# Kernel optimization log

Measured on AMD Instinct MI355X. Metric: run time of the kernel, lower is better.

## Reference

```python
import jax, jax.numpy as jnp
import numpy as np

NUM_SAMPLED = 8192
NUM_CLASSES = 50000
DIM = 512
BATCH = 8192


def _log_uniform_expected(ids, num_sampled, num_classes):
    # log-uniform sampler probability: P(c) = (log(c+2) - log(c+1)) / log(V+1)
    c = ids.astype(jnp.float32)
    p = (jnp.log(c + 2.0) - jnp.log(c + 1.0)) / jnp.log(float(num_classes + 1))
    # expected count under unique sampling of num_sampled candidates (as in TF)
    return -jnp.expm1(float(num_sampled) * jnp.log1p(-p))


def setup_inputs() -> dict:
    key = jax.random.key(0)
    k1, k2, k3, k4, k5 = jax.random.split(key, 5)
    inputs = jax.random.normal(k1, (BATCH, DIM), jnp.float32)
    labels = jax.random.randint(k2, (BATCH, 1), 0, NUM_CLASSES)
    kernel = jax.random.uniform(k3, (NUM_CLASSES, DIM), jnp.float32, -0.05, 0.05)
    bias = jax.random.uniform(k4, (NUM_CLASSES,), jnp.float32, -0.05, 0.05)
    sampled = jax.random.randint(k5, (NUM_SAMPLED,), 0, NUM_CLASSES)
    return {"inputs": inputs, "labels": labels, "kernel": kernel,
            "bias": bias, "sampled": sampled}


def reference(inputs, labels, kernel, bias, sampled):
    # tf.nn.sampled_softmax_loss (train branch), num_true=1,
    # log-uniform sampler, remove_accidental_hits=True.
    labels_flat = labels[:, 0]

    # true logits: gather one weight row per example, dot with input
    w_true = kernel[labels_flat]                      # [B, D]
    b_true = bias[labels_flat]                        # [B]
    true_logits = jnp.einsum('bd,bd->b', inputs, w_true) + b_true
    true_logits = true_logits - jnp.log(
        _log_uniform_expected(labels_flat, NUM_SAMPLED, NUM_CLASSES))

    # sampled logits: gather S candidate rows, small matmul [B,D]x[D,S]
    w_samp = kernel[sampled]                          # [S, D]
    b_samp = bias[sampled]                            # [S]
    sampled_logits = jnp.einsum('bd,sd->bs', inputs, w_samp) + b_samp[None, :]
    sampled_logits = sampled_logits - jnp.log(
        _log_uniform_expected(sampled, NUM_SAMPLED, NUM_CLASSES))

    # remove accidental hits: mask sampled candidates that equal the true label
    hits = labels_flat[:, None] == sampled[None, :]   # [B, S]
    sampled_logits = jnp.where(hits, -1e9, sampled_logits)

    # softmax CE with the true class at column 0
    logits = jnp.concatenate([true_logits[:, None], sampled_logits], axis=1)
    loss = jax.nn.logsumexp(logits, axis=1) - logits[:, 0]  # [B]
    return loss
```

## Files before the change

kernel.cpp:

```cpp
#include <hip/hip_runtime.h>
#include <hip/hip_bf16.h>
#include <cstdint>
#include <cstddef>

#define BATCH   8192
#define NSAMP   8192
#define DIM     512
#define NCLASS  50000

typedef __attribute__((ext_vector_type(8))) short bf16x8;
typedef __attribute__((ext_vector_type(4))) float f32x4;

__device__ __forceinline__ float neg_log_expected(int c) {
    double p = log1p(1.0 / (double)(c + 1)) / log((double)(NCLASS + 1));
    double e = -expm1((double)NSAMP * log1p(-p));
    return (float)(-log(e));
}

__device__ __forceinline__ unsigned short f2bf(float f) {
    __hip_bfloat16 h = __float2bfloat16(f);
    return *reinterpret_cast<unsigned short*>(&h);
}

__device__ __forceinline__ void gload_lds16(const void* g, void* l) {
    __builtin_amdgcn_global_load_lds(
        (const __attribute__((address_space(1))) void*)g,
        (__attribute__((address_space(3))) void*)l, 16, 0, 0);
}

__global__ void k_convert(const float* __restrict__ in, __hip_bfloat16* __restrict__ out) {
    int t = blockIdx.x * blockDim.x + threadIdx.x;
    float4 v = reinterpret_cast<const float4*>(in)[t];
    ushort4 u;
    u.x = f2bf(v.x); u.y = f2bf(v.y); u.z = f2bf(v.z); u.w = f2bf(v.w);
    reinterpret_cast<ushort4*>(out)[t] = u;
}

__global__ void k_gather(const float* __restrict__ W, const float* __restrict__ bias,
                         const int* __restrict__ sampled,
                         __hip_bfloat16* __restrict__ Bbf, float* __restrict__ adj) {
    int s   = blockIdx.x;
    int idx = sampled[s];
    const float4* src = reinterpret_cast<const float4*>(W + (size_t)idx * DIM);
    float4 v = src[threadIdx.x];
    ushort4 u;
    u.x = f2bf(v.x); u.y = f2bf(v.y); u.z = f2bf(v.z); u.w = f2bf(v.w);
    reinterpret_cast<ushort4*>(Bbf + (size_t)s * DIM)[threadIdx.x] = u;
    if (threadIdx.x == 0) adj[s] = bias[idx] + neg_log_expected(idx);
}

__global__ void k_true(const float* __restrict__ inputs, const int* __restrict__ labels,
                       const float* __restrict__ W, const float* __restrict__ bias,
                       float* __restrict__ true_logit, float* __restrict__ row_sum) {
    int gt   = blockIdx.x * blockDim.x + threadIdx.x;
    int row  = gt >> 6;
    int lane = gt & 63;
    int lbl  = labels[row];
    const float4* xi = reinterpret_cast<const float4*>(inputs + (size_t)row * DIM);
    const float4* wi = reinterpret_cast<const float4*>(W + (size_t)lbl * DIM);
    float dot = 0.f;
    #pragma unroll
    for (int j = 0; j < 2; ++j) {
        float4 a = xi[lane + j * 64];
        float4 b = wi[lane + j * 64];
        dot += a.x * b.x + a.y * b.y + a.z * b.z + a.w * b.w;
    }
    #pragma unroll
    for (int off = 32; off; off >>= 1) dot += __shfl_down(dot, off, 64);
    if (lane == 0) {
        float tl = dot + bias[lbl] + neg_log_expected(lbl);
        true_logit[row] = tl;
        row_sum[row]    = expf(tl);
    }
}

__global__ __launch_bounds__(256) void k_gemm(
    const __hip_bfloat16* __restrict__ A, const __hip_bfloat16* __restrict__ B,
    const float* __restrict__ adj, const int* __restrict__ labels,
    const int* __restrict__ sampled, float* __restrict__ row_sum) {
    __shared__ alignas(16) __hip_bfloat16 Asm[3][128 * 32];
    __shared__ alignas(16) __hip_bfloat16 Bsm[3][128 * 32];
    __shared__ float tsum[2][128];

    const int tid  = threadIdx.x;
    const int wave = tid >> 6;
    const int lane = tid & 63;
    const int wr   = wave >> 1;
    const int wc   = wave & 1;

    int bid = blockIdx.x;
    int wg  = (bid & 7) * 512 + (bid >> 3);
    const int brow = (wg >> 6) * 128;
    const int bcol = (wg & 63) * 128;

    const int srow = lane >> 2;
    const int sg   = (lane & 3) ^ ((lane >> 3) & 3);

    f32x4 acc[4][4];
    #pragma unroll
    for (int m = 0; m < 4; ++m)
        #pragma unroll
        for (int n = 0; n < 4; ++n)
            acc[m][n] = (f32x4){0.f, 0.f, 0.f, 0.f};

    auto stage = [&](int buf, int kt) {
        #pragma unroll
        for (int i = 0; i < 2; ++i) {
            const __hip_bfloat16* gA =
                A + (size_t)(brow + wave * 32 + i * 16 + srow) * DIM + kt * 32 + sg * 8;
            gload_lds16(gA, &Asm[buf][(wave * 32 + i * 16) * 32]);
            const __hip_bfloat16* gB =
                B + (size_t)(bcol + wave * 32 + i * 16 + srow) * DIM + kt * 32 + sg * 8;
            gload_lds16(gB, &Bsm[buf][(wave * 32 + i * 16) * 32]);
        }
    };

    stage(0, 0);
    stage(1, 1);

    const int rsel = lane & 15;
    const int koff = ((lane >> 4) ^ ((lane >> 1) & 3)) * 8;

    bf16x8 a[4], b[4];
    #pragma unroll 1
    for (int kt = 0; kt < 15; ++kt) {
        asm volatile("s_waitcnt vmcnt(4)" ::: "memory");
        asm volatile("s_barrier" ::: "memory");
        const int cur = kt % 3;
        #pragma unroll
        for (int m = 0; m < 4; ++m)
            a[m] = *reinterpret_cast<const bf16x8*>(
                &Asm[cur][(wr * 64 + m * 16 + rsel) * 32 + koff]);
        #pragma unroll
        for (int n = 0; n < 4; ++n)
            b[n] = *reinterpret_cast<const bf16x8*>(
                &Bsm[cur][(wc * 64 + n * 16 + rsel) * 32 + koff]);
        if (kt < 14) stage((kt + 2) % 3, kt + 2);
        #pragma unroll
        for (int m = 0; m < 4; ++m)
            #pragma unroll
            for (int n = 0; n < 4; ++n)
                acc[m][n] = __builtin_amdgcn_mfma_f32_16x16x32_bf16(a[m], b[n], acc[m][n], 0, 0, 0);
    }
    {
        asm volatile("s_waitcnt vmcnt(0)" ::: "memory");
        asm volatile("s_barrier" ::: "memory");
        #pragma unroll
        for (int m = 0; m < 4; ++m)
            a[m] = *reinterpret_cast<const bf16x8*>(
                &Asm[0][(wr * 64 + m * 16 + rsel) * 32 + koff]);
        #pragma unroll
        for (int n = 0; n < 4; ++n)
            b[n] = *reinterpret_cast<const bf16x8*>(
                &Bsm[0][(wc * 64 + n * 16 + rsel) * 32 + koff]);
        #pragma unroll
        for (int m = 0; m < 4; ++m)
            #pragma unroll
            for (int n = 0; n < 4; ++n)
                acc[m][n] = __builtin_amdgcn_mfma_f32_16x16x32_bf16(a[m], b[n], acc[m][n], 0, 0, 0);
    }

    int gcol[4]; float aadj[4]; int sval[4];
    #pragma unroll
    for (int n = 0; n < 4; ++n) {
        gcol[n] = bcol + wc * 64 + n * 16 + rsel;
        aadj[n] = adj[gcol[n]];
        sval[n] = sampled[gcol[n]];
    }
    #pragma unroll
    for (int m = 0; m < 4; ++m) {
        #pragma unroll
        for (int r = 0; r < 4; ++r) {
            int lr  = wr * 64 + m * 16 + (lane >> 4) * 4 + r;
            int lbl = labels[brow + lr];
            float part = 0.f;
            #pragma unroll
            for (int n = 0; n < 4; ++n) {
                float logit = acc[m][n][r] + aadj[n];
                part += (sval[n] == lbl) ? 0.f : __expf(logit);
            }
            part += __shfl_xor(part, 1, 16);
            part += __shfl_xor(part, 2, 16);
            part += __shfl_xor(part, 4, 16);
            part += __shfl_xor(part, 8, 16);
            if (rsel == 0) tsum[wc][lr] = part;
        }
    }
    __syncthreads();
    if (tid < 128) atomicAdd(&row_sum[brow + tid], tsum[0][tid] + tsum[1][tid]);
}

__global__ void k_final(const float* __restrict__ row_sum,
                        const float* __restrict__ true_logit,
                        float* __restrict__ loss) {
    int i = blockIdx.x * blockDim.x + threadIdx.x;
    loss[i] = logf(row_sum[i]) - true_logit[i];
}

extern "C" void kernel_launch(void* const* d_in, const int* in_sizes, int n_in,
                              void* d_out, int out_size, void* d_ws, size_t ws_size,
                              hipStream_t stream) {
    const float* inputs  = (const float*)d_in[0];
    const int*   labels  = (const int*)d_in[1];
    const float* W       = (const float*)d_in[2];
    const float* bias    = (const float*)d_in[3];
    const int*   sampled = (const int*)d_in[4];
    float*       loss    = (float*)d_out;

    char* ws = (char*)d_ws;
    __hip_bfloat16* Abf = (__hip_bfloat16*)ws;
    __hip_bfloat16* Bbf = (__hip_bfloat16*)(ws + (size_t)BATCH * DIM * 2);
    float* adj        = (float*)(ws + (size_t)(BATCH + NSAMP) * DIM * 2);
    float* true_logit = adj + NSAMP;
    float* row_sum    = true_logit + BATCH;

    hipLaunchKernelGGL(k_convert, dim3((BATCH * DIM / 4) / 256), dim3(256), 0, stream,
                       inputs, Abf);
    hipLaunchKernelGGL(k_gather, dim3(NSAMP), dim3(128), 0, stream,
                       W, bias, sampled, Bbf, adj);
    hipLaunchKernelGGL(k_true, dim3(BATCH / 4), dim3(256), 0, stream,
                       inputs, labels, W, bias, true_logit, row_sum);
    hipLaunchKernelGGL(k_gemm, dim3((BATCH / 128) * (NSAMP / 128)), dim3(256), 0, stream,
                       Abf, Bbf, adj, labels, sampled, row_sum);
    hipLaunchKernelGGL(k_final, dim3(BATCH / 256), dim3(256), 0, stream,
                       row_sum, true_logit, loss);
}
```

Measured before the change: 147.3 us.

## Persistent GEMM over column tiles with 4-stage pipeline and fused convert/true-logit kernel

The GEMM becomes a persistent kernel with 512 blocks. Each block processes 8 consecutive column tiles for one row block, and the load pipeline runs continuously across tile boundaries with a 4-buffer ring. This removes per-tile prologue and epilogue stalls and launch overhead, and keeps A rows resident in cache per XCD. The input conversion and true-logit dot product are also fused into one kernel that reads inputs once. The cost is fewer blocks, so occupancy is lower (launch_bounds 256,2), and the epilogue now sits inside the main loop.

```diff
diff --git a/kernel.cpp b/kernel.cpp
--- a/kernel.cpp
+++ b/kernel.cpp
@@ -28,12 +28,30 @@
         (__attribute__((address_space(3))) void*)l, 16, 0, 0);
 }
 
-__global__ void k_convert(const float* __restrict__ in, __hip_bfloat16* __restrict__ out) {
-    int t = blockIdx.x * blockDim.x + threadIdx.x;
-    float4 v = reinterpret_cast<const float4*>(in)[t];
+__global__ void k_fused(const float* __restrict__ inputs, const int* __restrict__ labels,
+                        const float* __restrict__ W, const float* __restrict__ bias,
+                        __hip_bfloat16* __restrict__ Abf,
+                        float* __restrict__ true_logit, float* __restrict__ row_sum) {
+    int row = blockIdx.x;
+    int t   = threadIdx.x;
+    float4 v = reinterpret_cast<const float4*>(inputs + (size_t)row * DIM)[t];
     ushort4 u;
     u.x = f2bf(v.x); u.y = f2bf(v.y); u.z = f2bf(v.z); u.w = f2bf(v.w);
-    reinterpret_cast<ushort4*>(out)[t] = u;
+    reinterpret_cast<ushort4*>(Abf + (size_t)row * DIM)[t] = u;
+
+    int lbl = labels[row];
+    float4 w = reinterpret_cast<const float4*>(W + (size_t)lbl * DIM)[t];
+    float dot = v.x * w.x + v.y * w.y + v.z * w.z + v.w * w.w;
+    #pragma unroll
+    for (int off = 32; off; off >>= 1) dot += __shfl_down(dot, off, 64);
+    __shared__ float red[2];
+    if ((t & 63) == 0) red[t >> 6] = dot;
+    __syncthreads();
+    if (t == 0) {
+        float tl = red[0] + red[1] + bias[lbl] + neg_log_expected(lbl);
+        true_logit[row] = tl;
+        row_sum[row]    = __expf(tl);
+    }
 }
 
 __global__ void k_gather(const float* __restrict__ W, const float* __restrict__ bias,
@@ -41,45 +59,24 @@
                          __hip_bfloat16* __restrict__ Bbf, float* __restrict__ adj) {
     int s   = blockIdx.x;
     int idx = sampled[s];
-    const float4* src = reinterpret_cast<const float4*>(W + (size_t)idx * DIM);
-    float4 v = src[threadIdx.x];
+    float4 v = reinterpret_cast<const float4*>(W + (size_t)idx * DIM)[threadIdx.x];
     ushort4 u;
     u.x = f2bf(v.x); u.y = f2bf(v.y); u.z = f2bf(v.z); u.w = f2bf(v.w);
     reinterpret_cast<ushort4*>(Bbf + (size_t)s * DIM)[threadIdx.x] = u;
     if (threadIdx.x == 0) adj[s] = bias[idx] + neg_log_expected(idx);
 }
 
-__global__ void k_true(const float* __restrict__ inputs, const int* __restrict__ labels,
-                       const float* __restrict__ W, const float* __restrict__ bias,
-                       float* __restrict__ true_logit, float* __restrict__ row_sum) {
-    int gt   = blockIdx.x * blockDim.x + threadIdx.x;
-    int row  = gt >> 6;
-    int lane = gt & 63;
-    int lbl  = labels[row];
-    const float4* xi = reinterpret_cast<const float4*>(inputs + (size_t)row * DIM);
-    const float4* wi = reinterpret_cast<const float4*>(W + (size_t)lbl * DIM);
-    float dot = 0.f;
-    #pragma unroll
-    for (int j = 0; j < 2; ++j) {
-        float4 a = xi[lane + j * 64];
-        float4 b = wi[lane + j * 64];
-        dot += a.x * b.x + a.y * b.y + a.z * b.z + a.w * b.w;
-    }
-    #pragma unroll
-    for (int off = 32; off; off >>= 1) dot += __shfl_down(dot, off, 64);
-    if (lane == 0) {
-        float tl = dot + bias[lbl] + neg_log_expected(lbl);
-        true_logit[row] = tl;
-        row_sum[row]    = expf(tl);
-    }
-}
-
-__global__ __launch_bounds__(256) void k_gemm(
+
+#define BARRIER()  asm volatile("s_barrier" ::: "memory")
+#define LBARRIER() asm volatile("s_waitcnt lgkmcnt(0)\n\ts_barrier" ::: "memory")
+#define VMCNT(n)   asm volatile("s_waitcnt vmcnt(" #n ")" ::: "memory")
+
+__global__ __launch_bounds__(256, 2) void k_gemm(
     const __hip_bfloat16* __restrict__ A, const __hip_bfloat16* __restrict__ B,
     const float* __restrict__ adj, const int* __restrict__ labels,
     const int* __restrict__ sampled, float* __restrict__ row_sum) {
-    __shared__ alignas(16) __hip_bfloat16 Asm[3][128 * 32];
-    __shared__ alignas(16) __hip_bfloat16 Bsm[3][128 * 32];
+    __shared__ alignas(16) __hip_bfloat16 Asm[4][128 * 32];
+    __shared__ alignas(16) __hip_bfloat16 Bsm[4][128 * 32];
     __shared__ float tsum[2][128];
 
     const int tid  = threadIdx.x;
@@ -88,13 +85,17 @@
     const int wr   = wave >> 1;
     const int wc   = wave & 1;
 
-    int bid = blockIdx.x;
-    int wg  = (bid & 7) * 512 + (bid >> 3);
-    const int brow = (wg >> 6) * 128;
-    const int bcol = (wg & 63) * 128;
+    const int bid  = blockIdx.x;
+    const int xcd  = bid & 7;
+    const int idx  = bid >> 3;
+    const int rb   = (idx & 7) * 8 + xcd;
+    const int cg   = idx >> 3;
+    const int brow = rb * 128;
 
     const int srow = lane >> 2;
     const int sg   = (lane & 3) ^ ((lane >> 3) & 3);
+    const int rsel = lane & 15;
+    const int koff = ((lane >> 4) ^ ((lane >> 1) & 3)) * 8;
 
     f32x4 acc[4][4];
     #pragma unroll
@@ -103,7 +104,9 @@
         for (int n = 0; n < 4; ++n)
             acc[m][n] = (f32x4){0.f, 0.f, 0.f, 0.f};
 
-    auto stage = [&](int buf, int kt) {
+    auto stage = [&](int g) {
+        const int buf = g & 3, t = g >> 4, kt = g & 15;
+        const int bcol = (cg * 8 + t) * 128;
         #pragma unroll
         for (int i = 0; i < 2; ++i) {
             const __hip_bfloat16* gA =
@@ -115,79 +118,75 @@
         }
     };
 
-    stage(0, 0);
-    stage(1, 1);
-
-    const int rsel = lane & 15;
-    const int koff = ((lane >> 4) ^ ((lane >> 1) & 3)) * 8;
-
-    bf16x8 a[4], b[4];
-    #pragma unroll 1
-    for (int kt = 0; kt < 15; ++kt) {
-        asm volatile("s_waitcnt vmcnt(4)" ::: "memory");
-        asm volatile("s_barrier" ::: "memory");
-        const int cur = kt % 3;
+    auto body = [&](int buf) {
+        bf16x8 a[4], b[4];
         #pragma unroll
         for (int m = 0; m < 4; ++m)
             a[m] = *reinterpret_cast<const bf16x8*>(
-                &Asm[cur][(wr * 64 + m * 16 + rsel) * 32 + koff]);
+                &Asm[buf][(wr * 64 + m * 16 + rsel) * 32 + koff]);
         #pragma unroll
         for (int n = 0; n < 4; ++n)
             b[n] = *reinterpret_cast<const bf16x8*>(
-                &Bsm[cur][(wc * 64 + n * 16 + rsel) * 32 + koff]);
-        if (kt < 14) stage((kt + 2) % 3, kt + 2);
+                &Bsm[buf][(wc * 64 + n * 16 + rsel) * 32 + koff]);
         #pragma unroll
         for (int m = 0; m < 4; ++m)
             #pragma unroll
             for (int n = 0; n < 4; ++n)
                 acc[m][n] = __builtin_amdgcn_mfma_f32_16x16x32_bf16(a[m], b[n], acc[m][n], 0, 0, 0);
-    }
-    {
-        asm volatile("s_waitcnt vmcnt(0)" ::: "memory");
-        asm volatile("s_barrier" ::: "memory");
-        #pragma unroll
-        for (int m = 0; m < 4; ++m)
-            a[m] = *reinterpret_cast<const bf16x8*>(
-                &Asm[0][(wr * 64 + m * 16 + rsel) * 32 + koff]);
-        #pragma unroll
-        for (int n = 0; n < 4; ++n)
-            b[n] = *reinterpret_cast<const bf16x8*>(
-                &Bsm[0][(wc * 64 + n * 16 + rsel) * 32 + koff]);
+    };
+
+    auto epi = [&](int t) {
+        const int bcol = (cg * 8 + t) * 128;
+        int sv[4]; float aadj[4];
+        #pragma unroll
+        for (int n = 0; n < 4; ++n) {
+            int col = bcol + wc * 64 + n * 16 + rsel;
+            aadj[n] = adj[col];
+            sv[n]   = sampled[col];
+        }
+        #pragma unroll
+        for (int m = 0; m < 4; ++m) {
+            #pragma unroll
+            for (int r = 0; r < 4; ++r) {
+                int lr  = wr * 64 + m * 16 + (lane >> 4) * 4 + r;
+                int lbl = labels[brow + lr];
+                float part = 0.f;
+                #pragma unroll
+                for (int n = 0; n < 4; ++n) {
+                    float logit = acc[m][n][r] + aadj[n];
+                    part += (sv[n] == lbl) ? 0.f : __expf(logit);
+                }
+                part += __shfl_xor(part, 1, 16);
+                part += __shfl_xor(part, 2, 16);
+                part += __shfl_xor(part, 4, 16);
+                part += __shfl_xor(part, 8, 16);
+                if (rsel == 0) tsum[wc][lr] = part;
+            }
+        }
+        LBARRIER();
+        if (tid < 128)
+            atomicAdd(&row_sum[brow + tid], tsum[0][tid] + tsum[1][tid]);
         #pragma unroll
         for (int m = 0; m < 4; ++m)
             #pragma unroll
             for (int n = 0; n < 4; ++n)
-                acc[m][n] = __builtin_amdgcn_mfma_f32_16x16x32_bf16(a[m], b[n], acc[m][n], 0, 0, 0);
+                acc[m][n] = (f32x4){0.f, 0.f, 0.f, 0.f};
+    };
+
+    stage(0); stage(1); stage(2);
+
+    #pragma unroll 1
+    for (int g = 0; g < 126; ++g) {
+        VMCNT(8);
+        BARRIER();
+        const int buf = g & 3;
+        if (g + 3 < 128) stage(g + 3);
+        body(buf);
+        if ((g & 15) == 15) epi(g >> 4);
     }
-
-    int gcol[4]; float aadj[4]; int sval[4];
-    #pragma unroll
-    for (int n = 0; n < 4; ++n) {
-        gcol[n] = bcol + wc * 64 + n * 16 + rsel;
-        aadj[n] = adj[gcol[n]];
-        sval[n] = sampled[gcol[n]];
-    }
-    #pragma unroll
-    for (int m = 0; m < 4; ++m) {
-        #pragma unroll
-        for (int r = 0; r < 4; ++r) {
-            int lr  = wr * 64 + m * 16 + (lane >> 4) * 4 + r;
-            int lbl = labels[brow + lr];
-            float part = 0.f;
-            #pragma unroll
-            for (int n = 0; n < 4; ++n) {
-                float logit = acc[m][n][r] + aadj[n];
-                part += (sval[n] == lbl) ? 0.f : __expf(logit);
-            }
-            part += __shfl_xor(part, 1, 16);
-            part += __shfl_xor(part, 2, 16);
-            part += __shfl_xor(part, 4, 16);
-            part += __shfl_xor(part, 8, 16);
-            if (rsel == 0) tsum[wc][lr] = part;
-        }
-    }
-    __syncthreads();
-    if (tid < 128) atomicAdd(&row_sum[brow + tid], tsum[0][tid] + tsum[1][tid]);
+    VMCNT(4); BARRIER(); body(2);
+    VMCNT(0); BARRIER(); body(3);
+    epi(7);
 }
 
 __global__ void k_final(const float* __restrict__ row_sum,
@@ -214,13 +213,11 @@
     float* true_logit = adj + NSAMP;
     float* row_sum    = true_logit + BATCH;
 
-    hipLaunchKernelGGL(k_convert, dim3((BATCH * DIM / 4) / 256), dim3(256), 0, stream,
-                       inputs, Abf);
+    hipLaunchKernelGGL(k_fused, dim3(BATCH), dim3(128), 0, stream,
+                       inputs, labels, W, bias, Abf, true_logit, row_sum);
     hipLaunchKernelGGL(k_gather, dim3(NSAMP), dim3(128), 0, stream,
                        W, bias, sampled, Bbf, adj);
-    hipLaunchKernelGGL(k_true, dim3(BATCH / 4), dim3(256), 0, stream,
-                       inputs, labels, W, bias, true_logit, row_sum);
-    hipLaunchKernelGGL(k_gemm, dim3((BATCH / 128) * (NSAMP / 128)), dim3(256), 0, stream,
+    hipLaunchKernelGGL(k_gemm, dim3(512), dim3(256), 0, stream,
                        Abf, Bbf, adj, labels, sampled, row_sum);
     hipLaunchKernelGGL(k_final, dim3(BATCH / 256), dim3(256), 0, stream,
                        row_sum, true_logit, loss);
```

Result: no change. 148.9 us (+1.1%).
